# Optimization experiments

Hardware: AMD Instinct MI355X
Metric: run time of the kernel (lower is better)

The kernel has to match this reference:

```python
import jax, jax.numpy as jnp
import numpy as np

KH, KW, PAD = 32, 32, 10  # kernel_size and padding from NeuralMem.__init__


def setup_inputs() -> dict:
    key = jax.random.key(0)
    k1, k2, k3, k4 = jax.random.split(key, 4)
    image = jax.random.normal(k1, (64, 64, 3), dtype=jnp.float32)
    mem = jax.random.normal(k2, (8192, 3072), dtype=jnp.float32)    # faiss IndexFlatL2 bank (keys)
    mem2 = jax.random.normal(k3, (8192, 3072), dtype=jnp.float32)   # faiss reconstruction bank (values)
    mapping = jax.random.randint(k4, (8192,), 0, 8192)              # Counter.most_common(1) vote table
    return {"image": image, "mem": mem, "mem2": mem2, "mapping": mapping}


def reference(image, mem, mem2, mapping):
    H, W, C = image.shape
    x = image.transpose(2, 0, 1)                       # [C,H,W]  (permute(2,0,1))
    xp = jnp.pad(x, ((0, 0), (PAD, PAD), (PAD, PAD)))  # unfold padding
    Lh = H + 2 * PAD - KH + 1
    Lw = W + 2 * PAD - KW + 1
    ii = jnp.arange(Lh)[:, None] + jnp.arange(KH)[None, :]  # [Lh,KH]
    jj = jnp.arange(Lw)[:, None] + jnp.arange(KW)[None, :]  # [Lw,KW]
    # unfold: patches [C,Lh,KH,Lw,KW] -> [L, C*KH*KW] with torch's (C,kh,kw) column order
    patches = xp[:, ii[:, :, None, None], jj[None, None, :, :]]
    patches = patches.transpose(1, 3, 0, 2, 4).reshape(Lh * Lw, C * KH * KW)  # [L,D]
    # L2 kNN (k=1): argmin ||p - m||^2 = argmin (||m||^2 - 2 p.m); ||p||^2 is constant per row
    mem_sq = jnp.sum(mem * mem, axis=1)                # [N]
    scores = patches @ mem.T                           # [L,N]
    nn = jnp.argmin(mem_sq[None, :] - 2.0 * scores, axis=1)  # [L]
    # counter majority vote -> mem2 reconstruct
    recon = mem2[mapping[nn]]                          # [L,D]
    # fold (sum of overlapping patches), then crop padding
    rp = recon.reshape(Lh, Lw, C, KH, KW).transpose(2, 0, 3, 1, 4)  # [C,Lh,KH,Lw,KW]
    outp = jnp.zeros_like(xp).at[:, ii[:, :, None, None], jj[None, None, :, :]].add(rp)
    out = outp[:, PAD:PAD + H, PAD:PAD + W]            # [C,H,W]
    out = out / jnp.max(out)                           # out / out.flatten().max()
    return out.transpose(1, 2, 0)                      # [H,W,C]
```

## Files before the change

### kernel.cpp

```cpp
#include <hip/hip_runtime.h>

typedef unsigned short u16;
typedef unsigned int   u32;
typedef int      i32x4  __attribute__((ext_vector_type(4)));
typedef float    f32x4  __attribute__((ext_vector_type(4)));
typedef _Float16 f16x8  __attribute__((ext_vector_type(8)));

#define LHW   53
#define NP    2809
#define KDIM  3072
#define NMEM  8192
#define PADW  84
#define IMG   64
#define MPAD  2816
#define BIGF  3.402823466e+38f
#define MARGIN 24.0f
#define QS    31.75f
#define C2    (2.0f / (QS * QS))

#define O_XP    0UL
#define O_MSQ   84736UL
#define O_MI8   117504UL
#define O_AI8   25283328UL
#define O_D     33934080UL
#define O_PVAL  80071424UL
#define O_THR   81513216UL
#define O_ROWI  81524480UL
#define O_PART  81535744UL
#define O_ACC   83245312UL
#define WS_NEED3 83294464UL

#define F_XP    0
#define F_MSQ   21504
#define F_PVAL  29696
#define F_PIDX  119584
#define F_ROW   209472
#define F_ACC   212288
#define F_MAX   224576
#define NSPL    32
#define NRANGE  (NMEM / NSPL)

__device__ inline char q8(float x) {
    float y = x * QS;
    y = fminf(fmaxf(y, -127.f), 127.f);
    return (char)__float2int_rn(y);
}

__global__ void k_xp(const float* __restrict__ image, float* __restrict__ xp) {
    int id = blockIdx.x * 256 + threadIdx.x;
    if (id < 3 * PADW * PADW) {
        int c = id / (PADW * PADW), rem = id % (PADW * PADW);
        int py = rem / PADW, px = rem % PADW;
        float v = 0.f;
        if (py >= 10 && py < 74 && px >= 10 && px < 74)
            v = image[((py - 10) * IMG + (px - 10)) * 3 + c];
        xp[id] = v;
    }
}

__global__ __launch_bounds__(1024) void k_maxnorm(const float* __restrict__ acc,
                                                  float* __restrict__ out) {
    int t = threadIdx.x;
    float m = -BIGF;
    for (int i = t; i < 12288; i += 1024) m = fmaxf(m, acc[i]);
    #pragma unroll
    for (int s = 1; s < 64; s <<= 1) m = fmaxf(m, __shfl_xor(m, s));
    __shared__ float ls[16];
    int lane = t & 63, w = t >> 6;
    if (lane == 0) ls[w] = m;
    __syncthreads();
    float mv = ls[0];
    #pragma unroll
    for (int i = 1; i < 16; ++i) mv = fmaxf(mv, ls[i]);
    for (int i = t; i < 12288; i += 1024) {
        int c = i >> 12, y = (i >> 6) & 63, x = i & 63;
        out[(y * IMG + x) * 3 + c] = acc[i] / mv;
    }
}

__global__ __launch_bounds__(256) void k_quantmsq(const float* __restrict__ mem,
                                                  char* __restrict__ mq,
                                                  float* __restrict__ msq) {
    int j = blockIdx.x, t = threadIdx.x;
    const float4* r4 = (const float4*)(mem + (size_t)j * KDIM);
    char4* q4 = (char4*)(mq + (size_t)j * KDIM);
    float s = 0.f;
    #pragma unroll
    for (int i = 0; i < 3; ++i) {
        int idx = i * 256 + t;
        float4 v = r4[idx];
        s += v.x * v.x + v.y * v.y + v.z * v.z + v.w * v.w;
        char4 q = {q8(v.x), q8(v.y), q8(v.z), q8(v.w)};
        q4[idx] = q;
    }
    #pragma unroll
    for (int m = 1; m < 64; m <<= 1) s += __shfl_xor(s, m);
    __shared__ float ls[4];
    int lane = t & 63, w = t >> 6;
    if (lane == 0) ls[w] = s;
    __syncthreads();
    if (t == 0) msq[j] = ls[0] + ls[1] + ls[2] + ls[3];
}

__global__ __launch_bounds__(256) void k_quant_A(const float* __restrict__ xp,
                                                 char* __restrict__ aq) {
    int id = blockIdx.x * 256 + threadIdx.x;
    int e0 = id * 4;
    int p = e0 / KDIM, k = e0 - p * KDIM;
    char4 q = {0, 0, 0, 0};
    if (p < NP) {
        int c = k >> 10, kh = (k >> 5) & 31, kw = k & 31;
        int lh = p / LHW, lw = p - lh * LHW;
        const float* src = xp + c * (PADW * PADW) + (lh + kh) * PADW + lw + kw;
        q.x = q8(src[0]); q.y = q8(src[1]); q.z = q8(src[2]); q.w = q8(src[3]);
    }
    ((char4*)aq)[id] = q;
}

__global__ __launch_bounds__(256) void k_gemm_i8(
    const char* __restrict__ Aq, const char* __restrict__ Bq,
    const float* __restrict__ msq, _Float16* __restrict__ Dm,
    float* __restrict__ pval)
{
    __shared__ __align__(16) char lds[65536];
    const int t = threadIdx.x;
    const int lane = t & 63;
    const int w = t >> 6, wm = w >> 1, wn = w & 1;
    const int mrow = lane & 15;

    int L = blockIdx.x;
    int logical = (L & 7) * 176 + (L >> 3);
    int by = logical / 22, bx = logical - by * 22;
    const int rowBase = bx * 128;
    const int jBase   = by * 128;

    const int lrow = lane >> 3;
    const int gsrc = (lane & 7) ^ lrow;
    const char* gpl[8];
    unsigned ldsb[8];
    #pragma unroll
    for (int s = 0; s < 8; ++s) {
        int P = s >> 2, sub = s & 3;
        int row = sub * 32 + w * 8 + lrow;
        const char* basep = (P == 0 ? Aq : Bq);
        int gRow = (P == 0 ? rowBase : jBase) + row;
        gpl[s]  = basep + (size_t)gRow * KDIM + gsrc * 16;
        ldsb[s] = P * 16384 + (unsigned)(sub * 32 + w * 8) * 128;
    }

    i32x4 acc[4][4];
    #pragma unroll
    for (int i = 0; i < 4; ++i)
        #pragma unroll
        for (int j = 0; j < 4; ++j) { i32x4 z = {0, 0, 0, 0}; acc[i][j] = z; }

    #pragma unroll
    for (int s = 0; s < 8; ++s)
        __builtin_amdgcn_global_load_lds(
            (const __attribute__((address_space(1))) void*)(gpl[s]),
            (__attribute__((address_space(3))) void*)(lds + ldsb[s]),
            16, 0, 0);

    for (int kc = 0; kc < 24; ++kc) {
        const int cb = kc & 1;
        __syncthreads();
        if (kc < 23) {
            const unsigned nb = (cb ^ 1) * 32768u;
            #pragma unroll
            for (int s = 0; s < 8; ++s)
                __builtin_amdgcn_global_load_lds(
                    (const __attribute__((address_space(1))) void*)(gpl[s] + (kc + 1) * 128),
                    (__attribute__((address_space(3))) void*)(lds + nb + ldsb[s]),
                    16, 0, 0);
        }
        const char* lbase = lds + cb * 32768;
        #pragma unroll
        for (int kh2 = 0; kh2 < 2; ++kh2) {
            const int grp = kh2 * 4 + (lane >> 4);
            i32x4 ah[4];
            #pragma unroll
            for (int f = 0; f < 4; ++f) {
                int ra = wm * 64 + f * 16 + mrow;
                ah[f] = *(const i32x4*)(lbase + ra * 128 + (grp ^ (ra & 7)) * 16);
            }
            #pragma unroll
            for (int fj = 0; fj < 4; ++fj) {
                int rb = wn * 64 + fj * 16 + mrow;
                i32x4 bh = *(const i32x4*)(lbase + 16384 + rb * 128 + (grp ^ (rb & 7)) * 16);
                #pragma unroll
                for (int fi = 0; fi < 4; ++fi)
                    acc[fi][fj] = __builtin_amdgcn_mfma_i32_16x16x64_i8(ah[fi], bh, acc[fi][fj], 0, 0, 0);
            }
        }
    }

    float ms[4];
    #pragma unroll
    for (int fj = 0; fj < 4; ++fj) ms[fj] = msq[jBase + wn * 64 + fj * 16 + mrow] - 3072.0f;
    const int splitId = by * 2 + wn;
    #pragma unroll
    for (int fi = 0; fi < 4; ++fi) {
        #pragma unroll
        for (int r = 0; r < 4; ++r) {
            int p = rowBase + wm * 64 + fi * 16 + (lane >> 4) * 4 + r;
            float bv = BIGF;
            #pragma unroll
            for (int fj = 0; fj < 4; ++fj) {
                int j = jBase + wn * 64 + fj * 16 + mrow;
                float d = fmaf(-C2, (float)acc[fi][fj][r], ms[fj]);
                Dm[(size_t)p * NMEM + j] = (_Float16)d;
                bv = fminf(bv, d);
            }
            #pragma unroll
            for (int m = 1; m < 16; m <<= 1) bv = fminf(bv, __shfl_xor(bv, m));
            if (mrow == 0 && p < NP)
                pval[(size_t)p * 128 + splitId] = bv;
        }
    }
}

__global__ void k_thr(const float* __restrict__ pval, float* __restrict__ thr) {
    int p = blockIdx.x * 256 + threadIdx.x;
    if (p < NP) {
        const float4* v4 = (const float4*)(pval + (size_t)p * 128);
        float m = BIGF;
        #pragma unroll
        for (int i = 0; i < 32; ++i) {
            float4 v = v4[i];
            m = fminf(m, fminf(fminf(v.x, v.y), fminf(v.z, v.w)));
        }
        thr[p] = m + (MARGIN + 0.5f);
    }
}

__global__ __launch_bounds__(256) void k_refine(
    const _Float16* __restrict__ Dm, const float* __restrict__ thrv,
    const float* __restrict__ msq, const float* __restrict__ xp,
    const float* __restrict__ mem, const int* __restrict__ mapping,
    int* __restrict__ rowIdx)
{
    const int p = blockIdx.x, t = threadIdx.x;
    const _Float16* row = Dm + (size_t)p * NMEM;
    const int lane = t & 63, w = t >> 6;

    __shared__ float wred[4];
    __shared__ int cnt;
    __shared__ int cand[128];
    if (t == 0) cnt = 0;
    __syncthreads();
    const float th = thrv[p];

    #pragma unroll
    for (int i0 = 0; i0 < 4; ++i0) {
        int base = i0 * 2048 + t * 8;
        f16x8 v = *(const f16x8*)(row + base);
        #pragma unroll
        for (int e = 0; e < 8; ++e)
            if ((float)v[e] <= th) {
                int sl = atomicAdd(&cnt, 1);
                if (sl < 128) cand[sl] = base + e;
            }
    }
    __syncthreads();
    int n = min(cnt, 128);

    const int lh = p / LHW, lw = p - (p / LHW) * LHW;
    float bd = BIGF; int bj = 0x7fffffff;
    __shared__ float tot;
    for (int ci = 0; ci < n; ++ci) {
        int j = cand[ci];
        const float* mrow2 = mem + (size_t)j * KDIM;
        float s = 0.f;
        for (int k = t; k < KDIM; k += 256) {
            int c = k >> 10, kh = (k >> 5) & 31, kw = k & 31;
            s += xp[c * (PADW * PADW) + (lh + kh) * PADW + lw + kw] * mrow2[k];
        }
        #pragma unroll
        for (int m = 1; m < 64; m <<= 1) s += __shfl_xor(s, m);
        if (lane == 0) wred[w] = s;
        __syncthreads();
        if (t == 0) tot = wred[0] + wred[1] + wred[2] + wred[3];
        __syncthreads();
        float d = msq[j] - 2.f * tot;
        if (d < bd || (d == bd && j < bj)) { bd = d; bj = j; }
    }
    if (t == 0) rowIdx[p] = mapping[bj];
}

__global__ __launch_bounds__(256) void k_scatter(const float* __restrict__ mem2,
                                                 const int* __restrict__ rowIdx,
                                                 float* __restrict__ partial) {
    const int lh = blockIdx.x / 3, c = blockIdx.x % 3;
    __shared__ float accs[32 * 85];
    __shared__ int r2s[53];
    const int t = threadIdx.x;
    for (int i = t; i < 32 * 85; i += 256) accs[i] = 0.f;
    if (t < 53) r2s[t] = rowIdx[lh * LHW + t];
    __syncthreads();
    const int kh  = t >> 3;
    const int kwb = (t & 7) * 4;
    const size_t coff = (size_t)c * 1024 + kh * 32 + kwb;
    float* a0 = accs + kh * 85 + kwb;
    for (int lw = 0; lw < 53; ++lw) {
        const float4 v = *(const float4*)(mem2 + (size_t)r2s[lw] * KDIM + coff);
        float* a = a0 + lw;
        a[0] += v.x; a[1] += v.y; a[2] += v.z; a[3] += v.w;
        __syncthreads();
    }
    float* pbase = partial + ((size_t)(lh * 3 + c)) * 32 * 84;
    for (int i = t; i < 32 * 84; i += 256) {
        int kh2 = i / 84, px = i - kh2 * 84;
        pbase[i] = accs[kh2 * 85 + px];
    }
}

__global__ void k_oadd(const float* __restrict__ partial, float* __restrict__ accb) {
    int id = blockIdx.x * 256 + threadIdx.x;
    if (id >= 12288) return;
    int c = id >> 12, y = (id >> 6) & 63, x = id & 63;
    int py = y + 10, px = x + 10;
    int khmin = max(0, py - 52), khmax = min(31, py);
    float s = 0.f;
    for (int kh = khmin; kh <= khmax; ++kh) {
        int lh = py - kh;
        s += partial[((lh * 3 + c) * 32 + kh) * 84 + px];
    }
    accb[id] = s;
}

__global__ __launch_bounds__(256) void k_msq(const float* __restrict__ mem,
                                             float* __restrict__ msq) {
    int j = blockIdx.x;
    const float* row = mem + (size_t)j * KDIM;
    float s = 0.f;
    for (int i = threadIdx.x; i < KDIM; i += 256) { float v = row[i]; s += v * v; }
    #pragma unroll
    for (int m = 1; m < 64; m <<= 1) s += __shfl_xor(s, m);
    __shared__ float ls[4];
    int lane = threadIdx.x & 63, w = threadIdx.x >> 6;
    if (lane == 0) ls[w] = s;
    __syncthreads();
    if (threadIdx.x == 0) msq[j] = ls[0] + ls[1] + ls[2] + ls[3];
}

__global__ void k_amin(const float* __restrict__ pval, const int* __restrict__ pidx,
                       const int* __restrict__ mapping, int* __restrict__ rowIdx,
                       int nspl) {
    int p = blockIdx.x * 256 + threadIdx.x;
    if (p < NP) {
        float bv = BIGF; int bi = 0x7fffffff;
        for (int ns = 0; ns < nspl; ++ns) {
            float v = pval[(size_t)p * nspl + ns];
            int ix = pidx[(size_t)p * nspl + ns];
            if (v < bv || (v == bv && ix < bi)) { bv = v; bi = ix; }
        }
        rowIdx[p] = mapping[bi];
    }
}

__global__ __launch_bounds__(256) void k_gather(const float* __restrict__ mem2,
                                                const int* __restrict__ rowIdx,
                                                float* __restrict__ acc) {
    int b = blockIdx.x;
    int c = b >> 12, y = (b >> 6) & 63, x = b & 63;
    int khmin = max(0, y - 42), khmax = min(31, y + 10);
    int kwmin = max(0, x - 42), kwmax = min(31, x + 10);
    int nh = khmax - khmin + 1, nw = kwmax - kwmin + 1;
    int total = nh * nw;
    float s = 0.f;
    for (int idx = threadIdx.x; idx < total; idx += 256) {
        int kh = khmin + idx / nw;
        int kw = kwmin + idx % nw;
        int lh = y + 10 - kh, lw = x + 10 - kw;
        int p = lh * LHW + lw;
        int r2 = rowIdx[p];
        s += mem2[(size_t)r2 * KDIM + c * 1024 + kh * 32 + kw];
    }
    #pragma unroll
    for (int m = 1; m < 64; m <<= 1) s += __shfl_xor(s, m);
    __shared__ float ls[4];
    int lane = threadIdx.x & 63, w = threadIdx.x >> 6;
    if (lane == 0) ls[w] = s;
    __syncthreads();
    if (threadIdx.x == 0) acc[b] = ls[0] + ls[1] + ls[2] + ls[3];
}

__global__ __launch_bounds__(256) void k_gemm_argmin(
    const float* __restrict__ xp, const float* __restrict__ mem,
    const float* __restrict__ msq, float* __restrict__ pval,
    int* __restrict__ pidx)
{
    __shared__ float At[64][33];
    __shared__ float Bt[64][33];
    const int t = threadIdx.x;
    const int tx = t & 15, ty = t >> 4;
    const int rowBase = blockIdx.x * 64;
    const int nBase = blockIdx.y * NRANGE;

    float best[4]; int bidx[4];
    #pragma unroll
    for (int i = 0; i < 4; ++i) { best[i] = BIGF; bidx[i] = 0x7fffffff; }

    for (int nt = 0; nt < NRANGE / 64; ++nt) {
        const int jBase = nBase + nt * 64;
        float acc[4][4];
        #pragma unroll
        for (int i = 0; i < 4; ++i)
            #pragma unroll
            for (int j = 0; j < 4; ++j) acc[i][j] = 0.f;

        for (int kc = 0; kc < KDIM / 32; ++kc) {
            const int c = kc >> 5, kh = kc & 31;
            const float* xpc = xp + c * (PADW * PADW) + kh * PADW;
            #pragma unroll
            for (int i = 0; i < 8; ++i) {
                int e = i * 256 + t;
                int r = e >> 5, kwi = e & 31;
                int p = rowBase + r;
                float v = 0.f;
                if (p < NP) {
                    int lh = p / LHW, lw = p - lh * LHW;
                    v = xpc[lh * PADW + lw + kwi];
                }
                At[r][kwi] = v;
            }
            const float* mb = mem + (size_t)jBase * KDIM + kc * 32;
            #pragma unroll
            for (int i = 0; i < 8; ++i) {
                int e = i * 256 + t;
                int r = e >> 5, kwi = e & 31;
                Bt[r][kwi] = mb[(size_t)r * KDIM + kwi];
            }
            __syncthreads();
            #pragma unroll
            for (int kk = 0; kk < 32; ++kk) {
                float a[4], b[4];
                #pragma unroll
                for (int i = 0; i < 4; ++i) a[i] = At[ty + 16 * i][kk];
                #pragma unroll
                for (int j = 0; j < 4; ++j) b[j] = Bt[tx + 16 * j][kk];
                #pragma unroll
                for (int i = 0; i < 4; ++i)
                    #pragma unroll
                    for (int j = 0; j < 4; ++j) acc[i][j] += a[i] * b[j];
            }
            __syncthreads();
        }
        #pragma unroll
        for (int j = 0; j < 4; ++j) {
            int col = jBase + tx + 16 * j;
            float msv = msq[col];
            #pragma unroll
            for (int i = 0; i < 4; ++i) {
                float d = msv - 2.f * acc[i][j];
                if (d < best[i] || (d == best[i] && col < bidx[i])) {
                    best[i] = d; bidx[i] = col;
                }
            }
        }
    }
    #pragma unroll
    for (int m = 1; m < 16; m <<= 1) {
        #pragma unroll
        for (int i = 0; i < 4; ++i) {
            float ov = __shfl_xor(best[i], m);
            int   oi = __shfl_xor(bidx[i], m);
            if (ov < best[i] || (ov == best[i] && oi < bidx[i])) {
                best[i] = ov; bidx[i] = oi;
            }
        }
    }
    if (tx == 0) {
        #pragma unroll
        for (int i = 0; i < 4; ++i) {
            int p = rowBase + ty + 16 * i;
            if (p < NP) {
                pval[p * NSPL + blockIdx.y] = best[i];
                pidx[p * NSPL + blockIdx.y] = bidx[i];
            }
        }
    }
}

__global__ __launch_bounds__(256) void k_max(const float* __restrict__ acc,
                                             float* __restrict__ maxv) {
    float m = -BIGF;
    for (int i = threadIdx.x; i < 12288; i += 256) m = fmaxf(m, acc[i]);
    #pragma unroll
    for (int s = 1; s < 64; s <<= 1) m = fmaxf(m, __shfl_xor(m, s));
    __shared__ float ls[4];
    int lane = threadIdx.x & 63, w = threadIdx.x >> 6;
    if (lane == 0) ls[w] = m;
    __syncthreads();
    if (threadIdx.x == 0)
        maxv[0] = fmaxf(fmaxf(ls[0], ls[1]), fmaxf(ls[2], ls[3]));
}

__global__ void k_norm(const float* __restrict__ acc, const float* __restrict__ maxv,
                       float* __restrict__ out) {
    int id = blockIdx.x * 256 + threadIdx.x;
    if (id < 12288) {
        int c = id >> 12, y = (id >> 6) & 63, x = id & 63;
        out[(y * IMG + x) * 3 + c] = acc[id] / maxv[0];
    }
}

extern "C" void kernel_launch(void* const* d_in, const int* in_sizes, int n_in,
                              void* d_out, int out_size, void* d_ws, size_t ws_size,
                              hipStream_t stream) {
    const float* image   = (const float*)d_in[0];
    const float* mem     = (const float*)d_in[1];
    const float* mem2    = (const float*)d_in[2];
    const int*   mapping = (const int*)d_in[3];

    if (ws_size >= WS_NEED3) {
        char* wsB = (char*)d_ws;
        float*    xp   = (float*)(wsB + O_XP);
        float*    msq  = (float*)(wsB + O_MSQ);
        char*     mI8  = (char*)(wsB + O_MI8);
        char*     aI8  = (char*)(wsB + O_AI8);
        _Float16* Dm   = (_Float16*)(wsB + O_D);
        float*    pval = (float*)(wsB + O_PVAL);
        float*    thr  = (float*)(wsB + O_THR);
        int*      rowI = (int*)(wsB + O_ROWI);
        float*    part = (float*)(wsB + O_PART);
        float*    accb = (float*)(wsB + O_ACC);

        k_xp<<<dim3((3 * PADW * PADW + 255) / 256), 256, 0, stream>>>(image, xp);
        k_quantmsq<<<dim3(NMEM), 256, 0, stream>>>(mem, mI8, msq);
        k_quant_A<<<dim3(MPAD * KDIM / 4 / 256), 256, 0, stream>>>(xp, aI8);
        k_gemm_i8<<<dim3(1408), 256, 0, stream>>>(aI8, mI8, msq, Dm, pval);
        k_thr<<<dim3((NP + 255) / 256), 256, 0, stream>>>(pval, thr);
        k_refine<<<dim3(NP), 256, 0, stream>>>(Dm, thr, msq, xp, mem, mapping, rowI);
        k_scatter<<<dim3(LHW * 3), 256, 0, stream>>>(mem2, rowI, part);
        k_oadd<<<dim3(48), 256, 0, stream>>>(part, accb);
        k_maxnorm<<<dim3(1), 1024, 0, stream>>>(accb, (float*)d_out);
    } else {
        float* ws   = (float*)d_ws;
        float* xp   = ws + F_XP;
        float* msq  = ws + F_MSQ;
        float* pval = ws + F_PVAL;
        int*   pidx = (int*)(ws + F_PIDX);
        int*   rowI = (int*)(ws + F_ROW);
        float* acc  = ws + F_ACC;
        float* maxv = ws + F_MAX;

        k_xp<<<dim3((3 * PADW * PADW + 255) / 256), 256, 0, stream>>>(image, xp);
        k_msq<<<dim3(NMEM), 256, 0, stream>>>(mem, msq);
        k_gemm_argmin<<<dim3((NP + 63) / 64, NSPL), 256, 0, stream>>>(xp, mem, msq, pval, pidx);
        k_amin<<<dim3((NP + 255) / 256), 256, 0, stream>>>(pval, pidx, mapping, rowI, NSPL);
        k_gather<<<dim3(3 * IMG * IMG), 256, 0, stream>>>(mem2, rowI, acc);
        k_max<<<dim3(1), 256, 0, stream>>>(acc, maxv);
        k_norm<<<dim3((12288 + 255) / 256), 256, 0, stream>>>(acc, maxv, (float*)d_out);
    }
}
```

Measured before the change: 213.6 us.

## Emit per-split candidate lists from int8 GEMM instead of full fp16 distance matrix

```diff
diff --git a/kernel.cpp b/kernel.cpp
--- a/kernel.cpp
+++ b/kernel.cpp
@@ -4,7 +4,6 @@
 typedef unsigned int   u32;
 typedef int      i32x4  __attribute__((ext_vector_type(4)));
 typedef float    f32x4  __attribute__((ext_vector_type(4)));
-typedef _Float16 f16x8  __attribute__((ext_vector_type(8)));
 
 #define LHW   53
 #define NP    2809
@@ -17,18 +16,19 @@
 #define MARGIN 24.0f
 #define QS    31.75f
 #define C2    (2.0f / (QS * QS))
+#define CAP   12
 
 #define O_XP    0UL
 #define O_MSQ   84736UL
 #define O_MI8   117504UL
 #define O_AI8   25283328UL
-#define O_D     33934080UL
-#define O_PVAL  80071424UL
-#define O_THR   81513216UL
-#define O_ROWI  81524480UL
-#define O_PART  81535744UL
-#define O_ACC   83245312UL
-#define WS_NEED3 83294464UL
+#define O_CANDD 33934080UL
+#define O_CANDJ 51192576UL
+#define O_CNT   68451072UL
+#define O_ROWI  69889280UL
+#define O_PART  69900544UL
+#define O_ACC   71610112UL
+#define WS_NEED4 71659264UL
 
 #define F_XP    0
 #define F_MSQ   21504
@@ -103,8 +103,10 @@
 }
 
 __global__ __launch_bounds__(256) void k_quant_A(const float* __restrict__ xp,
-                                                 char* __restrict__ aq) {
+                                                 char* __restrict__ aq,
+                                                 int* __restrict__ cnt) {
     int id = blockIdx.x * 256 + threadIdx.x;
+    if (id < NP * 128) cnt[id] = 0;
     int e0 = id * 4;
     int p = e0 / KDIM, k = e0 - p * KDIM;
     char4 q = {0, 0, 0, 0};
@@ -119,8 +121,8 @@
 
 __global__ __launch_bounds__(256) void k_gemm_i8(
     const char* __restrict__ Aq, const char* __restrict__ Bq,
-    const float* __restrict__ msq, _Float16* __restrict__ Dm,
-    float* __restrict__ pval)
+    const float* __restrict__ msq, float* __restrict__ candd,
+    int* __restrict__ candj, int* __restrict__ cnt)
 {
     __shared__ __align__(16) char lds[65536];
     const int t = threadIdx.x;
@@ -203,72 +205,75 @@
         #pragma unroll
         for (int r = 0; r < 4; ++r) {
             int p = rowBase + wm * 64 + fi * 16 + (lane >> 4) * 4 + r;
-            float bv = BIGF;
+            float d4[4]; float bv = BIGF;
             #pragma unroll
             for (int fj = 0; fj < 4; ++fj) {
-                int j = jBase + wn * 64 + fj * 16 + mrow;
-                float d = fmaf(-C2, (float)acc[fi][fj][r], ms[fj]);
-                Dm[(size_t)p * NMEM + j] = (_Float16)d;
-                bv = fminf(bv, d);
+                d4[fj] = fmaf(-C2, (float)acc[fi][fj][r], ms[fj]);
+                bv = fminf(bv, d4[fj]);
             }
             #pragma unroll
             for (int m = 1; m < 16; m <<= 1) bv = fminf(bv, __shfl_xor(bv, m));
-            if (mrow == 0 && p < NP)
-                pval[(size_t)p * 128 + splitId] = bv;
-        }
-    }
-}
-
-__global__ void k_thr(const float* __restrict__ pval, float* __restrict__ thr) {
-    int p = blockIdx.x * 256 + threadIdx.x;
-    if (p < NP) {
-        const float4* v4 = (const float4*)(pval + (size_t)p * 128);
-        float m = BIGF;
-        #pragma unroll
-        for (int i = 0; i < 32; ++i) {
-            float4 v = v4[i];
-            m = fminf(m, fminf(fminf(v.x, v.y), fminf(v.z, v.w)));
-        }
-        thr[p] = m + (MARGIN + 0.5f);
+            if (p < NP) {
+                float th = bv + MARGIN;
+                int* cp = cnt + (size_t)p * 128 + splitId;
+                #pragma unroll
+                for (int fj = 0; fj < 4; ++fj) {
+                    if (d4[fj] <= th) {
+                        int slot = atomicAdd(cp, 1);
+                        if (slot < CAP) {
+                            size_t off = ((size_t)p * 128 + splitId) * CAP + slot;
+                            candd[off] = d4[fj];
+                            candj[off] = jBase + wn * 64 + fj * 16 + mrow;
+                        }
+                    }
+                }
+            }
+        }
     }
 }
 
 __global__ __launch_bounds__(256) void k_refine(
-    const _Float16* __restrict__ Dm, const float* __restrict__ thrv,
-    const float* __restrict__ msq, const float* __restrict__ xp,
-    const float* __restrict__ mem, const int* __restrict__ mapping,
-    int* __restrict__ rowIdx)
+    const float* __restrict__ candd, const int* __restrict__ candj,
+    const int* __restrict__ cnt, const float* __restrict__ msq,
+    const float* __restrict__ xp, const float* __restrict__ mem,
+    const int* __restrict__ mapping, int* __restrict__ rowIdx)
 {
     const int p = blockIdx.x, t = threadIdx.x;
-    const _Float16* row = Dm + (size_t)p * NMEM;
     const int lane = t & 63, w = t >> 6;
-
     __shared__ float wred[4];
-    __shared__ int cnt;
-    __shared__ int cand[128];
-    if (t == 0) cnt = 0;
-    __syncthreads();
-    const float th = thrv[p];
-
-    #pragma unroll
-    for (int i0 = 0; i0 < 4; ++i0) {
-        int base = i0 * 2048 + t * 8;
-        f16x8 v = *(const f16x8*)(row + base);
-        #pragma unroll
-        for (int e = 0; e < 8; ++e)
-            if ((float)v[e] <= th) {
-                int sl = atomicAdd(&cnt, 1);
-                if (sl < 128) cand[sl] = base + e;
-            }
-    }
-    __syncthreads();
-    int n = min(cnt, 128);
+    __shared__ int lcnt;
+    __shared__ int list[256];
+    __shared__ float thr_s;
+
+    int n = 0;
+    if (t < 128) n = min(cnt[(size_t)p * 128 + t], CAP);
+    const float* dp = candd + ((size_t)p * 128 + t) * CAP;
+    const int*   jp = candj + ((size_t)p * 128 + t) * CAP;
+
+    float gm = BIGF;
+    for (int i = 0; i < n; ++i) gm = fminf(gm, dp[i]);
+    #pragma unroll
+    for (int m = 1; m < 64; m <<= 1) gm = fminf(gm, __shfl_xor(gm, m));
+    if (lane == 0) wred[w] = gm;
+    if (t == 0) lcnt = 0;
+    __syncthreads();
+    if (t == 0) thr_s = fminf(fminf(wred[0], wred[1]), fminf(wred[2], wred[3])) + MARGIN;
+    __syncthreads();
+    const float th = thr_s;
+
+    for (int i = 0; i < n; ++i)
+        if (dp[i] <= th) {
+            int sl = atomicAdd(&lcnt, 1);
+            if (sl < 256) list[sl] = jp[i];
+        }
+    __syncthreads();
+    int nc = min(lcnt, 256);
 
     const int lh = p / LHW, lw = p - (p / LHW) * LHW;
     float bd = BIGF; int bj = 0x7fffffff;
     __shared__ float tot;
-    for (int ci = 0; ci < n; ++ci) {
-        int j = cand[ci];
+    for (int ci = 0; ci < nc; ++ci) {
+        int j = list[ci];
         const float* mrow2 = mem + (size_t)j * KDIM;
         float s = 0.f;
         for (int k = t; k < KDIM; k += 256) {
@@ -513,25 +518,24 @@
     const float* mem2    = (const float*)d_in[2];
     const int*   mapping = (const int*)d_in[3];
 
-    if (ws_size >= WS_NEED3) {
+    if (ws_size >= WS_NEED4) {
         char* wsB = (char*)d_ws;
-        float*    xp   = (float*)(wsB + O_XP);
-        float*    msq  = (float*)(wsB + O_MSQ);
-        char*     mI8  = (char*)(wsB + O_MI8);
-        char*     aI8  = (char*)(wsB + O_AI8);
-        _Float16* Dm   = (_Float16*)(wsB + O_D);
-        float*    pval = (float*)(wsB + O_PVAL);
-        float*    thr  = (float*)(wsB + O_THR);
-        int*      rowI = (int*)(wsB + O_ROWI);
-        float*    part = (float*)(wsB + O_PART);
-        float*    accb = (float*)(wsB + O_ACC);
+        float*    xp    = (float*)(wsB + O_XP);
+        float*    msq   = (float*)(wsB + O_MSQ);
+        char*     mI8   = (char*)(wsB + O_MI8);
+        char*     aI8   = (char*)(wsB + O_AI8);
+        float*    candd = (float*)(wsB + O_CANDD);
+        int*      candj = (int*)(wsB + O_CANDJ);
+        int*      cnt   = (int*)(wsB + O_CNT);
+        int*      rowI  = (int*)(wsB + O_ROWI);
+        float*    part  = (float*)(wsB + O_PART);
+        float*    accb  = (float*)(wsB + O_ACC);
 
         k_xp<<<dim3((3 * PADW * PADW + 255) / 256), 256, 0, stream>>>(image, xp);
         k_quantmsq<<<dim3(NMEM), 256, 0, stream>>>(mem, mI8, msq);
-        k_quant_A<<<dim3(MPAD * KDIM / 4 / 256), 256, 0, stream>>>(xp, aI8);
-        k_gemm_i8<<<dim3(1408), 256, 0, stream>>>(aI8, mI8, msq, Dm, pval);
-        k_thr<<<dim3((NP + 255) / 256), 256, 0, stream>>>(pval, thr);
-        k_refine<<<dim3(NP), 256, 0, stream>>>(Dm, thr, msq, xp, mem, mapping, rowI);
+        k_quant_A<<<dim3(MPAD * KDIM / 4 / 256), 256, 0, stream>>>(xp, aI8, cnt);
+        k_gemm_i8<<<dim3(1408), 256, 0, stream>>>(aI8, mI8, msq, candd, candj, cnt);
+        k_refine<<<dim3(NP), 256, 0, stream>>>(candd, candj, cnt, msq, xp, mem, mapping, rowI);
         k_scatter<<<dim3(LHW * 3), 256, 0, stream>>>(mem2, rowI, part);
         k_oadd<<<dim3(48), 256, 0, stream>>>(part, accb);
         k_maxnorm<<<dim3(1), 1024, 0, stream>>>(accb, (float*)d_out);
```

New measurement: 264.8 us. +24.0%, slower.

## Fuse threshold into refine and scatter-add directly into output accumulator

Applied to the files above, without the earlier changes.

```diff
diff --git a/kernel.cpp b/kernel.cpp
--- a/kernel.cpp
+++ b/kernel.cpp
@@ -2,6 +2,7 @@
 
 typedef unsigned short u16;
 typedef unsigned int   u32;
+typedef unsigned long long u64;
 typedef int      i32x4  __attribute__((ext_vector_type(4)));
 typedef float    f32x4  __attribute__((ext_vector_type(4)));
 typedef _Float16 f16x8  __attribute__((ext_vector_type(8)));
@@ -24,11 +25,9 @@
 #define O_AI8   25283328UL
 #define O_D     33934080UL
 #define O_PVAL  80071424UL
-#define O_THR   81513216UL
 #define O_ROWI  81524480UL
-#define O_PART  81535744UL
-#define O_ACC   83245312UL
-#define WS_NEED3 83294464UL
+#define O_ACC   81535744UL
+#define WS_NEED5 81584896UL
 
 #define F_XP    0
 #define F_MSQ   21504
@@ -46,8 +45,10 @@
     return (char)__float2int_rn(y);
 }
 
-__global__ void k_xp(const float* __restrict__ image, float* __restrict__ xp) {
+__global__ void k_xp(const float* __restrict__ image, float* __restrict__ xp,
+                     float* __restrict__ accb) {
     int id = blockIdx.x * 256 + threadIdx.x;
+    if (id < 12288) accb[id] = 0.f;
     if (id < 3 * PADW * PADW) {
         int c = id / (PADW * PADW), rem = id % (PADW * PADW);
         int py = rem / PADW, px = rem % PADW;
@@ -219,22 +220,8 @@
     }
 }
 
-__global__ void k_thr(const float* __restrict__ pval, float* __restrict__ thr) {
-    int p = blockIdx.x * 256 + threadIdx.x;
-    if (p < NP) {
-        const float4* v4 = (const float4*)(pval + (size_t)p * 128);
-        float m = BIGF;
-        #pragma unroll
-        for (int i = 0; i < 32; ++i) {
-            float4 v = v4[i];
-            m = fminf(m, fminf(fminf(v.x, v.y), fminf(v.z, v.w)));
-        }
-        thr[p] = m + (MARGIN + 0.5f);
-    }
-}
-
 __global__ __launch_bounds__(256) void k_refine(
-    const _Float16* __restrict__ Dm, const float* __restrict__ thrv,
+    const _Float16* __restrict__ Dm, const float* __restrict__ pval,
     const float* __restrict__ msq, const float* __restrict__ xp,
     const float* __restrict__ mem, const int* __restrict__ mapping,
     int* __restrict__ rowIdx)
@@ -244,11 +231,21 @@
     const int lane = t & 63, w = t >> 6;
 
     __shared__ float wred[4];
-    __shared__ int cnt;
-    __shared__ int cand[128];
-    if (t == 0) cnt = 0;
-    __syncthreads();
-    const float th = thrv[p];
+    __shared__ int lcnt;
+    __shared__ int list[256];
+    __shared__ float thr_s;
+
+    float pm = (t < 128) ? pval[(size_t)p * 128 + t] : BIGF;
+    #pragma unroll
+    for (int m = 1; m < 64; m <<= 1) pm = fminf(pm, __shfl_xor(pm, m));
+    if (lane == 0) wred[w] = pm;
+    if (t == 0) lcnt = 0;
+    __syncthreads();
+    if (t == 0)
+        thr_s = fminf(fminf(wred[0], wred[1]), fminf(wred[2], wred[3]))
+                + (MARGIN + 0.5f);
+    __syncthreads();
+    const float th = thr_s;
 
     #pragma unroll
     for (int i0 = 0; i0 < 4; ++i0) {
@@ -257,18 +254,18 @@
         #pragma unroll
         for (int e = 0; e < 8; ++e)
             if ((float)v[e] <= th) {
-                int sl = atomicAdd(&cnt, 1);
-                if (sl < 128) cand[sl] = base + e;
-            }
-    }
-    __syncthreads();
-    int n = min(cnt, 128);
+                int sl = atomicAdd(&lcnt, 1);
+                if (sl < 256) list[sl] = base + e;
+            }
+    }
+    __syncthreads();
+    int nc = min(lcnt, 256);
 
     const int lh = p / LHW, lw = p - (p / LHW) * LHW;
     float bd = BIGF; int bj = 0x7fffffff;
     __shared__ float tot;
-    for (int ci = 0; ci < n; ++ci) {
-        int j = cand[ci];
+    for (int ci = 0; ci < nc; ++ci) {
+        int j = list[ci];
         const float* mrow2 = mem + (size_t)j * KDIM;
         float s = 0.f;
         for (int k = t; k < KDIM; k += 256) {
@@ -289,7 +286,7 @@
 
 __global__ __launch_bounds__(256) void k_scatter(const float* __restrict__ mem2,
                                                  const int* __restrict__ rowIdx,
-                                                 float* __restrict__ partial) {
+                                                 float* __restrict__ accb) {
     const int lh = blockIdx.x / 3, c = blockIdx.x % 3;
     __shared__ float accs[32 * 85];
     __shared__ int r2s[53];
@@ -307,25 +304,12 @@
         a[0] += v.x; a[1] += v.y; a[2] += v.z; a[3] += v.w;
         __syncthreads();
     }
-    float* pbase = partial + ((size_t)(lh * 3 + c)) * 32 * 84;
     for (int i = t; i < 32 * 84; i += 256) {
         int kh2 = i / 84, px = i - kh2 * 84;
-        pbase[i] = accs[kh2 * 85 + px];
-    }
-}
-
-__global__ void k_oadd(const float* __restrict__ partial, float* __restrict__ accb) {
-    int id = blockIdx.x * 256 + threadIdx.x;
-    if (id >= 12288) return;
-    int c = id >> 12, y = (id >> 6) & 63, x = id & 63;
-    int py = y + 10, px = x + 10;
-    int khmin = max(0, py - 52), khmax = min(31, py);
-    float s = 0.f;
-    for (int kh = khmin; kh <= khmax; ++kh) {
-        int lh = py - kh;
-        s += partial[((lh * 3 + c) * 32 + kh) * 84 + px];
-    }
-    accb[id] = s;
+        int y = lh + kh2 - 10, x = px - 10;
+        if (y >= 0 && y < 64 && x >= 0 && x < 64)
+            atomicAdd(&accb[c * 4096 + y * 64 + x], accs[kh2 * 85 + px]);
+    }
 }
 
 __global__ __launch_bounds__(256) void k_msq(const float* __restrict__ mem,
@@ -513,7 +497,7 @@
     const float* mem2    = (const float*)d_in[2];
     const int*   mapping = (const int*)d_in[3];
 
-    if (ws_size >= WS_NEED3) {
+    if (ws_size >= WS_NEED5) {
         char* wsB = (char*)d_ws;
         float*    xp   = (float*)(wsB + O_XP);
         float*    msq  = (float*)(wsB + O_MSQ);
@@ -521,19 +505,15 @@
         char*     aI8  = (char*)(wsB + O_AI8);
         _Float16* Dm   = (_Float16*)(wsB + O_D);
         float*    pval = (float*)(wsB + O_PVAL);
-        float*    thr  = (float*)(wsB + O_THR);
         int*      rowI = (int*)(wsB + O_ROWI);
-        float*    part = (float*)(wsB + O_PART);
         float*    accb = (float*)(wsB + O_ACC);
 
-        k_xp<<<dim3((3 * PADW * PADW + 255) / 256), 256, 0, stream>>>(image, xp);
+        k_xp<<<dim3((3 * PADW * PADW + 255) / 256), 256, 0, stream>>>(image, xp, accb);
         k_quantmsq<<<dim3(NMEM), 256, 0, stream>>>(mem, mI8, msq);
         k_quant_A<<<dim3(MPAD * KDIM / 4 / 256), 256, 0, stream>>>(xp, aI8);
         k_gemm_i8<<<dim3(1408), 256, 0, stream>>>(aI8, mI8, msq, Dm, pval);
-        k_thr<<<dim3((NP + 255) / 256), 256, 0, stream>>>(pval, thr);
-        k_refine<<<dim3(NP), 256, 0, stream>>>(Dm, thr, msq, xp, mem, mapping, rowI);
-        k_scatter<<<dim3(LHW * 3), 256, 0, stream>>>(mem2, rowI, part);
-        k_oadd<<<dim3(48), 256, 0, stream>>>(part, accb);
+        k_refine<<<dim3(NP), 256, 0, stream>>>(Dm, pval, msq, xp, mem, mapping, rowI);
+        k_scatter<<<dim3(LHW * 3), 256, 0, stream>>>(mem2, rowI, accb);
         k_maxnorm<<<dim3(1), 1024, 0, stream>>>(accb, (float*)d_out);
     } else {
         float* ws   = (float*)d_ws;
@@ -545,7 +525,7 @@
         float* acc  = ws + F_ACC;
         float* maxv = ws + F_MAX;
 
-        k_xp<<<dim3((3 * PADW * PADW + 255) / 256), 256, 0, stream>>>(image, xp);
+        k_xp<<<dim3((3 * PADW * PADW + 255) / 256), 256, 0, stream>>>(image, xp, acc);
         k_msq<<<dim3(NMEM), 256, 0, stream>>>(mem, msq);
         k_gemm_argmin<<<dim3((NP + 63) / 64, NSPL), 256, 0, stream>>>(xp, mem, msq, pval, pidx);
         k_amin<<<dim3((NP + 255) / 256), 256, 0, stream>>>(pval, pidx, mapping, rowI, NSPL);
```

New measurement: 199.0 us. -6.8%, faster.
